# Kernel optimization log

Measured on AMD Instinct MI355X. Metric: run time of the kernel, lower is better.

Reference implementation:

```python
import jax, jax.numpy as jnp
import numpy as np

LOGIT_SCALE = 1.0 / 0.07  # from ClipLoss(temperature=0.07)


def setup_inputs() -> dict:
    key = jax.random.key(0)
    k1, k2 = jax.random.split(key)
    N, D = 16384, 512
    return {
        "image_features": jax.random.normal(k1, (N, D), dtype=jnp.float32),
        "text_features": jax.random.normal(k2, (N, D), dtype=jnp.float32),
    }


def reference(image_features, text_features):
    # logits_per_image[i, j] = scale * <img_i, txt_j>; logits_per_text is its transpose
    logits_per_image = LOGIT_SCALE * (image_features @ text_features.T)  # [N, N]
    logits_per_text = logits_per_image.T
    n = logits_per_image.shape[0]
    labels = jnp.arange(n)
    # cross_entropy(logits, labels) = mean over rows of (logsumexp(row) - row[label])
    def ce(logits):
        logp = jax.nn.log_softmax(logits, axis=-1)
        return -jnp.mean(jnp.take_along_axis(logp, labels[:, None], axis=-1))
    return (ce(logits_per_image) + ce(logits_per_text)) / 2.0
```

## Files before the change

### kernel.cpp

```cpp
#include <hip/hip_runtime.h>
#include <cstdint>
#include <cstddef>
#include <cmath>


#define N_ROWS 16384
#define DIM    512
#define NB     128
#define SCALE  14.285714285714286f
#define CF     20.609929155556625f
#define LN2F   0.6931471805599453f
#define SP     36

typedef __attribute__((ext_vector_type(8))) int   int8v;
typedef __attribute__((ext_vector_type(4))) int   int4v;
typedef __attribute__((ext_vector_type(4))) float floatx4;

#if __has_builtin(__builtin_amdgcn_exp2f)
#define EXP2(x) __builtin_amdgcn_exp2f(x)
#else
#define EXP2(x) exp2f(x)
#endif

__device__ __forceinline__ void async_load16(const void* g, void* l) {
    __builtin_amdgcn_global_load_lds(
        (__attribute__((address_space(1))) void*)(void*)(g),
        (__attribute__((address_space(3))) void*)(l), 16, 0, 0);
}

__device__ __forceinline__ void lse_merge2(float& m, float& s, float om, float os) {
    float nm = fmaxf(m, om);
    s = s * EXP2(m - nm) + os * EXP2(om - nm);
    m = nm;
}

__device__ __forceinline__ int pk_fp8x4(float a, float b, float c, float d) {
    int u = __builtin_amdgcn_cvt_pk_fp8_f32(a, b, 0, false);
    u = __builtin_amdgcn_cvt_pk_fp8_f32(c, d, u, true);
    return u;
}

__global__ void cvt_diag_kernel(const float* __restrict__ a, const float* __restrict__ b,
                                unsigned char* __restrict__ A8, unsigned char* __restrict__ B8,
                                float* __restrict__ diag) {
    const int t  = threadIdx.x;
    const int rl = t & 15, g16 = t >> 4;
    const int row = blockIdx.x * 16 + rl;
    const float4* ai = (const float4*)(a + (size_t)row * DIM + g16 * 32);
    const float4* bi = (const float4*)(b + (size_t)row * DIM + g16 * 32);
    float dot = 0.f;
    int wa[8], wb[8];
#pragma unroll
    for (int j = 0; j < 4; ++j) {
        float4 x0 = ai[2 * j], x1 = ai[2 * j + 1];
        float4 y0 = bi[2 * j], y1 = bi[2 * j + 1];
        dot += x0.x * y0.x + x0.y * y0.y + x0.z * y0.z + x0.w * y0.w
             + x1.x * y1.x + x1.y * y1.y + x1.z * y1.z + x1.w * y1.w;
        wa[2 * j]     = pk_fp8x4(CF * x0.x, CF * x0.y, CF * x0.z, CF * x0.w);
        wa[2 * j + 1] = pk_fp8x4(CF * x1.x, CF * x1.y, CF * x1.z, CF * x1.w);
        wb[2 * j]     = pk_fp8x4(y0.x, y0.y, y0.z, y0.w);
        wb[2 * j + 1] = pk_fp8x4(y1.x, y1.y, y1.z, y1.w);
    }
    const size_t o = ((size_t)g16 * N_ROWS + row) * 32;
    *(int4v*)(A8 + o)      = (int4v){wa[0], wa[1], wa[2], wa[3]};
    *(int4v*)(A8 + o + 16) = (int4v){wa[4], wa[5], wa[6], wa[7]};
    *(int4v*)(B8 + o)      = (int4v){wb[0], wb[1], wb[2], wb[3]};
    *(int4v*)(B8 + o + 16) = (int4v){wb[4], wb[5], wb[6], wb[7]};

    __shared__ float pd[16][17];
    pd[rl][g16] = dot;
    __syncthreads();
    if (t < 16) {
        float s = 0.f;
#pragma unroll
        for (int j = 0; j < 16; ++j) s += pd[t][j];
        diag[blockIdx.x * 16 + t] = SCALE * s;
    }
}

__global__ void gemm_lse_kernel(const unsigned char* __restrict__ A8,
                                const unsigned char* __restrict__ B8,
                                float* __restrict__ row_m, float* __restrict__ row_s,
                                float* __restrict__ col_m, float* __restrict__ col_s) {
    __shared__ __align__(16) unsigned char smem[32768];
    unsigned char* sA = smem;
    unsigned char* sB = smem + 16384;
    float* part = (float*)smem;

    const int t = threadIdx.x;
    const int bid = blockIdx.x;

    const int xcd   = bid & 7;
    const int local = bid >> 3;
    const int br    = xcd * 16 + (local & 15);
    const int bc    = local >> 4;

    const int lane = t & 63;
    const int w    = t >> 6;
    const int quad = lane >> 4;
    const int l15  = lane & 15;
    const int wrow = w >> 1;
    const int wcol = w & 1;

    floatx4 acc[4][4];
#pragma unroll
    for (int i = 0; i < 4; ++i)
#pragma unroll
        for (int j = 0; j < 4; ++j)
            acc[i][j] = (floatx4){0.f, 0.f, 0.f, 0.f};

    const int isB   = w >> 1;
    const int gbase = (w & 1) * 2;
    const unsigned char* gsrc = isB ? B8 : A8;
    const int rbase = (isB ? bc : br) * 128;
    unsigned char* lbase = isB ? sB : sA;

    const unsigned char* gp[8];
    unsigned char* lp[8];
#pragma unroll
    for (int c = 0; c < 8; ++c) {
        const int g = gbase + (c >> 2), i = c & 3;
        gp[c] = gsrc + ((size_t)g * N_ROWS + rbase) * 32 + i * 1024 + lane * 16;
        lp[c] = lbase + g * 4096 + i * 1024;
    }
    const size_t kbstr = (size_t)4 * N_ROWS * 32;

    for (int kb = 0; kb < 4; ++kb) {
        const size_t ko = (size_t)kb * kbstr;
#pragma unroll
        for (int c = 0; c < 8; ++c) async_load16(gp[c] + ko, lp[c]);
        __builtin_amdgcn_s_waitcnt(0);
        __syncthreads();

        int8v av[4], bv[4];
#pragma unroll
        for (int mi = 0; mi < 4; ++mi) {
            const unsigned char* p = sA + (quad * 128 + wrow * 64 + mi * 16 + l15) * 32;
            int4v lo = *(const int4v*)p;
            int4v hi = *(const int4v*)(p + 16);
            av[mi] = (int8v){lo[0], lo[1], lo[2], lo[3], hi[0], hi[1], hi[2], hi[3]};
        }
#pragma unroll
        for (int ni = 0; ni < 4; ++ni) {
            const unsigned char* p = sB + (quad * 128 + wcol * 64 + ni * 16 + l15) * 32;
            int4v lo = *(const int4v*)p;
            int4v hi = *(const int4v*)(p + 16);
            bv[ni] = (int8v){lo[0], lo[1], lo[2], lo[3], hi[0], hi[1], hi[2], hi[3]};
        }
#pragma unroll
        for (int mi = 0; mi < 4; ++mi)
#pragma unroll
            for (int ni = 0; ni < 4; ++ni)
                acc[mi][ni] = __builtin_amdgcn_mfma_scale_f32_16x16x128_f8f6f4(
                    av[mi], bv[ni], acc[mi][ni], 0, 0, 0, 127, 0, 127);
        __syncthreads();
    }


#pragma unroll
    for (int mi = 0; mi < 4; ++mi)
#pragma unroll
        for (int r = 0; r < 4; ++r) {
            float pm = fmaxf(fmaxf(acc[mi][0][r], acc[mi][1][r]),
                             fmaxf(acc[mi][2][r], acc[mi][3][r]));
            int lrow = wrow * 64 + mi * 16 + quad * 4 + r;
            part[lrow * SP + wcol * 16 + l15] = pm;
        }

#pragma unroll
    for (int ni = 0; ni < 4; ++ni) {
        float m = acc[0][ni][0];
#pragma unroll
        for (int mi = 0; mi < 4; ++mi)
#pragma unroll
            for (int r = 0; r < 4; ++r)
                m = fmaxf(m, acc[mi][ni][r]);
        m = fmaxf(m, __shfl_xor(m, 16));
        m = fmaxf(m, __shfl_xor(m, 32));
        float s = 0.f;
#pragma unroll
        for (int mi = 0; mi < 4; ++mi)
#pragma unroll
            for (int r = 0; r < 4; ++r)
                s += EXP2(acc[mi][ni][r] - m);
        s += __shfl_xor(s, 16);
        s += __shfl_xor(s, 32);
        if (quad == 0) {
            int cl = wcol * 64 + ni * 16 + l15;
            part[cl * SP + 32 + wrow] = m;
            part[cl * SP + 34 + wrow] = s;
        }
    }
    __syncthreads();

    if (t < 128) {
        float m = part[t * SP + 32], s = part[t * SP + 34];
        lse_merge2(m, s, part[t * SP + 33], part[t * SP + 35]);
        col_m[(size_t)br * N_ROWS + bc * 128 + t] = m;
        col_s[(size_t)br * N_ROWS + bc * 128 + t] = s;
        const float4* p4 = (const float4*)&part[t * SP];
        float4 v = p4[0];
#pragma unroll
        for (int j = 1; j < 8; ++j) {
            float4 u = p4[j];
            v.x = fmaxf(v.x, u.x); v.y = fmaxf(v.y, u.y);
            v.z = fmaxf(v.z, u.z); v.w = fmaxf(v.w, u.w);
        }
        part[t * SP + 32] = fmaxf(fmaxf(v.x, v.y), fmaxf(v.z, v.w));
    }
    __syncthreads();

#pragma unroll
    for (int mi = 0; mi < 4; ++mi)
#pragma unroll
        for (int r = 0; r < 4; ++r) {
            int lrow = wrow * 64 + mi * 16 + quad * 4 + r;
            float m = part[lrow * SP + 32];
            float s = EXP2(acc[mi][0][r] - m) + EXP2(acc[mi][1][r] - m)
                    + EXP2(acc[mi][2][r] - m) + EXP2(acc[mi][3][r] - m);
            part[lrow * SP + wcol * 16 + l15] = s;
        }
    __syncthreads();

    if (t < 128) {
        const float4* p4 = (const float4*)&part[t * SP];
        float4 v = p4[0];
#pragma unroll
        for (int j = 1; j < 8; ++j) {
            float4 u = p4[j];
            v.x += u.x; v.y += u.y; v.z += u.z; v.w += u.w;
        }
        float s = (v.x + v.y) + (v.z + v.w);
        float m = part[t * SP + 32];
        row_m[(size_t)bc * N_ROWS + br * 128 + t] = m;
        row_s[(size_t)bc * N_ROWS + br * 128 + t] = s;
    }
}

__global__ void reduce_kernel(const float* __restrict__ row_m, const float* __restrict__ row_s,
                              const float* __restrict__ col_m, const float* __restrict__ col_s,
                              const float* __restrict__ diag, float* __restrict__ out) {
    const int w = threadIdx.x >> 6, lane = threadIdx.x & 63;
    const int row = blockIdx.x * 64 + lane;
    const size_t jt0 = (size_t)w * 32;

    float m = row_m[jt0 * N_ROWS + row];
    float s = row_s[jt0 * N_ROWS + row];
    for (int k = 1; k < 32; ++k)
        lse_merge2(m, s, row_m[(jt0 + k) * N_ROWS + row], row_s[(jt0 + k) * N_ROWS + row]);
    float mc = col_m[jt0 * N_ROWS + row];
    float sc = col_s[jt0 * N_ROWS + row];
    for (int k = 1; k < 32; ++k)
        lse_merge2(mc, sc, col_m[(jt0 + k) * N_ROWS + row], col_s[(jt0 + k) * N_ROWS + row]);

    __shared__ float sm[4][64], ss[4][64], tm[4][64], ts[4][64];
    sm[w][lane] = m;  ss[w][lane] = s;
    tm[w][lane] = mc; ts[w][lane] = sc;
    __syncthreads();

    if (w == 0) {
#pragma unroll
        for (int h = 1; h < 4; ++h) lse_merge2(m, s, sm[h][lane], ss[h][lane]);
        float lse_r = m + log2f(s);
#pragma unroll
        for (int h = 1; h < 4; ++h) lse_merge2(mc, sc, tm[h][lane], ts[h][lane]);
        float lse_c = mc + log2f(sc);
        float contrib = 0.5f * LN2F * (lse_r + lse_c) - diag[row];
        for (int mask = 32; mask; mask >>= 1) contrib += __shfl_xor(contrib, mask);
        if (lane == 0) atomicAdd(out, contrib * (1.0f / N_ROWS));
    }
}

extern "C" void kernel_launch(void* const* d_in, const int* in_sizes, int n_in,
                              void* d_out, int out_size, void* d_ws, size_t ws_size,
                              hipStream_t stream) {
    const float* img = (const float*)d_in[0];
    const float* txt = (const float*)d_in[1];
    char* ws = (char*)d_ws;

    const size_t MB = 1024 * 1024;
    unsigned char* A8 = (unsigned char*)(ws);
    unsigned char* B8 = (unsigned char*)(ws + 8 * MB);
    float* row_m = (float*)(ws + 16 * MB);
    float* row_s = (float*)(ws + 24 * MB);
    float* col_m = (float*)(ws + 32 * MB);
    float* col_s = (float*)(ws + 40 * MB);
    float* diag  = (float*)(ws + 48 * MB);
    float* out   = (float*)d_out;

    hipMemsetAsync(d_out, 0, sizeof(float), stream);
    cvt_diag_kernel<<<N_ROWS / 16, 256, 0, stream>>>(img, txt, A8, B8, diag);
    gemm_lse_kernel<<<NB * NB, 256, 0, stream>>>(A8, B8, row_m, row_s, col_m, col_s);
    reduce_kernel<<<N_ROWS / 64, 256, 0, stream>>>(row_m, row_s, col_m, col_s, diag, out);
}
```

Measured before the change: 329.3 us.

## Switch fp8 operand layout to 16-byte planes to cut LDS bank conflicts

```diff
diff --git a/kernel.cpp b/kernel.cpp
--- a/kernel.cpp
+++ b/kernel.cpp
@@ -11,6 +11,7 @@
 #define CF     20.609929155556625f
 #define LN2F   0.6931471805599453f
 #define SP     36
+#define CVP    528
 
 typedef __attribute__((ext_vector_type(8))) int   int8v;
 typedef __attribute__((ext_vector_type(4))) int   int4v;
@@ -43,38 +44,51 @@
 __global__ void cvt_diag_kernel(const float* __restrict__ a, const float* __restrict__ b,
                                 unsigned char* __restrict__ A8, unsigned char* __restrict__ B8,
                                 float* __restrict__ diag) {
-    const int t  = threadIdx.x;
-    const int rl = t & 15, g16 = t >> 4;
-    const int row = blockIdx.x * 16 + rl;
-    const float4* ai = (const float4*)(a + (size_t)row * DIM + g16 * 32);
-    const float4* bi = (const float4*)(b + (size_t)row * DIM + g16 * 32);
-    float dot = 0.f;
-    int wa[8], wb[8];
-#pragma unroll
-    for (int j = 0; j < 4; ++j) {
-        float4 x0 = ai[2 * j], x1 = ai[2 * j + 1];
-        float4 y0 = bi[2 * j], y1 = bi[2 * j + 1];
-        dot += x0.x * y0.x + x0.y * y0.y + x0.z * y0.z + x0.w * y0.w
-             + x1.x * y1.x + x1.y * y1.y + x1.z * y1.z + x1.w * y1.w;
-        wa[2 * j]     = pk_fp8x4(CF * x0.x, CF * x0.y, CF * x0.z, CF * x0.w);
-        wa[2 * j + 1] = pk_fp8x4(CF * x1.x, CF * x1.y, CF * x1.z, CF * x1.w);
-        wb[2 * j]     = pk_fp8x4(y0.x, y0.y, y0.z, y0.w);
-        wb[2 * j + 1] = pk_fp8x4(y1.x, y1.y, y1.z, y1.w);
-    }
-    const size_t o = ((size_t)g16 * N_ROWS + row) * 32;
-    *(int4v*)(A8 + o)      = (int4v){wa[0], wa[1], wa[2], wa[3]};
-    *(int4v*)(A8 + o + 16) = (int4v){wa[4], wa[5], wa[6], wa[7]};
-    *(int4v*)(B8 + o)      = (int4v){wb[0], wb[1], wb[2], wb[3]};
-    *(int4v*)(B8 + o + 16) = (int4v){wb[4], wb[5], wb[6], wb[7]};
-
-    __shared__ float pd[16][17];
-    pd[rl][g16] = dot;
-    __syncthreads();
-    if (t < 16) {
-        float s = 0.f;
-#pragma unroll
-        for (int j = 0; j < 16; ++j) s += pd[t][j];
-        diag[blockIdx.x * 16 + t] = SCALE * s;
+    __shared__ __align__(16) unsigned char la[16 * CVP];
+    __shared__ __align__(16) unsigned char lb[16 * CVP];
+    const int t = threadIdx.x;
+    const int rb = blockIdx.x * 16;
+
+    {
+        const int r = t >> 4, gg = t & 15;
+        const float4* ai = (const float4*)(a + (size_t)(rb + r) * DIM + gg * 32);
+        const float4* bi = (const float4*)(b + (size_t)(rb + r) * DIM + gg * 32);
+        float dot = 0.f;
+        int wa[8], wb[8];
+#pragma unroll
+        for (int j = 0; j < 4; ++j) {
+            float4 x0 = ai[2 * j], x1 = ai[2 * j + 1];
+            float4 y0 = bi[2 * j], y1 = bi[2 * j + 1];
+            dot += x0.x * y0.x + x0.y * y0.y + x0.z * y0.z + x0.w * y0.w
+                 + x1.x * y1.x + x1.y * y1.y + x1.z * y1.z + x1.w * y1.w;
+            wa[2 * j]     = pk_fp8x4(CF * x0.x, CF * x0.y, CF * x0.z, CF * x0.w);
+            wa[2 * j + 1] = pk_fp8x4(CF * x1.x, CF * x1.y, CF * x1.z, CF * x1.w);
+            wb[2 * j]     = pk_fp8x4(y0.x, y0.y, y0.z, y0.w);
+            wb[2 * j + 1] = pk_fp8x4(y1.x, y1.y, y1.z, y1.w);
+        }
+        *(int4v*)(la + r * CVP + gg * 32)      = (int4v){wa[0], wa[1], wa[2], wa[3]};
+        *(int4v*)(la + r * CVP + gg * 32 + 16) = (int4v){wa[4], wa[5], wa[6], wa[7]};
+        *(int4v*)(lb + r * CVP + gg * 32)      = (int4v){wb[0], wb[1], wb[2], wb[3]};
+        *(int4v*)(lb + r * CVP + gg * 32 + 16) = (int4v){wb[4], wb[5], wb[6], wb[7]};
+        dot += __shfl_xor(dot, 1);
+        dot += __shfl_xor(dot, 2);
+        dot += __shfl_xor(dot, 4);
+        dot += __shfl_xor(dot, 8);
+        if (gg == 0) diag[rb + r] = SCALE * dot;
+    }
+    __syncthreads();
+
+    {
+        const int row = t & 15;
+#pragma unroll
+        for (int hh = 0; hh < 2; ++hh) {
+            const int p = (t >> 4) + hh * 16;
+            int4v va = *(const int4v*)(la + row * CVP + p * 16);
+            int4v vb = *(const int4v*)(lb + row * CVP + p * 16);
+            const size_t o = ((size_t)p * N_ROWS + rb + row) * 16;
+            *(int4v*)(A8 + o) = va;
+            *(int4v*)(B8 + o) = vb;
+        }
     }
 }
 
@@ -110,7 +124,7 @@
             acc[i][j] = (floatx4){0.f, 0.f, 0.f, 0.f};
 
     const int isB   = w >> 1;
-    const int gbase = (w & 1) * 2;
+    const int pbase = (w & 1) * 4;
     const unsigned char* gsrc = isB ? B8 : A8;
     const int rbase = (isB ? bc : br) * 128;
     unsigned char* lbase = isB ? sB : sA;
@@ -119,11 +133,11 @@
     unsigned char* lp[8];
 #pragma unroll
     for (int c = 0; c < 8; ++c) {
-        const int g = gbase + (c >> 2), i = c & 3;
-        gp[c] = gsrc + ((size_t)g * N_ROWS + rbase) * 32 + i * 1024 + lane * 16;
-        lp[c] = lbase + g * 4096 + i * 1024;
-    }
-    const size_t kbstr = (size_t)4 * N_ROWS * 32;
+        const int pl = pbase + (c >> 1), rh = c & 1;
+        gp[c] = gsrc + ((size_t)pl * N_ROWS + rbase + rh * 64 + lane) * 16;
+        lp[c] = lbase + (pl * 128 + rh * 64) * 16;
+    }
+    const size_t kbstr = (size_t)8 * N_ROWS * 16;
 
     for (int kb = 0; kb < 4; ++kb) {
         const size_t ko = (size_t)kb * kbstr;
@@ -135,16 +149,16 @@
         int8v av[4], bv[4];
 #pragma unroll
         for (int mi = 0; mi < 4; ++mi) {
-            const unsigned char* p = sA + (quad * 128 + wrow * 64 + mi * 16 + l15) * 32;
-            int4v lo = *(const int4v*)p;
-            int4v hi = *(const int4v*)(p + 16);
+            const int row = wrow * 64 + mi * 16 + l15;
+            int4v lo = *(const int4v*)(sA + ((quad * 2) * 128 + row) * 16);
+            int4v hi = *(const int4v*)(sA + ((quad * 2 + 1) * 128 + row) * 16);
             av[mi] = (int8v){lo[0], lo[1], lo[2], lo[3], hi[0], hi[1], hi[2], hi[3]};
         }
 #pragma unroll
         for (int ni = 0; ni < 4; ++ni) {
-            const unsigned char* p = sB + (quad * 128 + wcol * 64 + ni * 16 + l15) * 32;
-            int4v lo = *(const int4v*)p;
-            int4v hi = *(const int4v*)(p + 16);
+            const int row = wcol * 64 + ni * 16 + l15;
+            int4v lo = *(const int4v*)(sB + ((quad * 2) * 128 + row) * 16);
+            int4v hi = *(const int4v*)(sB + ((quad * 2 + 1) * 128 + row) * 16);
             bv[ni] = (int8v){lo[0], lo[1], lo[2], lo[3], hi[0], hi[1], hi[2], hi[3]};
         }
 #pragma unroll
```

Measured after the change: 385.7 us. 1.17x slower.
